# Kernel optimization log

Hardware: AMD Instinct MI355X
Metric: run time of the kernel (lower is better)

The kernel has to match this reference:

```python
import jax, jax.numpy as jnp
import numpy as np

B, S, D = 1, 2048, 1024   # batch, seq, hidden_size
I = 2048                  # intermediate_size (mlp1 emits 2*I, SwiGLU halves)
E = 8                     # num_experts
K = 2                     # experts_per_token
LIMIT = 7.0               # swiglu_limit
ALPHA = 1.702             # gpt-oss swiglu alpha
EPS = 1e-5                # RMSNorm eps


def setup_inputs() -> dict:
    key = jax.random.key(0)
    ks = jax.random.split(key, 4)
    s = 0.02
    return {
        "x": jax.random.normal(ks[0], (B, S, D), jnp.float32),
        "norm_scale": jnp.ones((D,), jnp.float32),
        "gate_w": jax.random.normal(ks[1], (D, E), jnp.float32) * s,
        "gate_b": jnp.zeros((E,), jnp.float32),
        "mlp1_w": jax.random.normal(ks[2], (E, D, 2 * I), jnp.float32) * s,
        "mlp1_b": jnp.zeros((E, 2 * I), jnp.float32),
        "mlp2_w": jax.random.normal(ks[3], (E, I, D), jnp.float32) * s,
        "mlp2_b": jnp.zeros((E, D), jnp.float32),
    }


def _swiglu(h):
    # gpt-oss interleaved SwiGLU with clamp limit
    x_glu = jnp.minimum(h[..., ::2], LIMIT)
    x_lin = jnp.clip(h[..., 1::2], -LIMIT, LIMIT)
    return x_glu * jax.nn.sigmoid(ALPHA * x_glu) * (x_lin + 1.0)


def _moe(t, gate_w, gate_b, mlp1_w, mlp1_b, mlp2_w, mlp2_b):
    T = t.shape[0]
    logits = t @ gate_w + gate_b                 # [T, E]
    top_v, top_i = jax.lax.top_k(logits, K)      # [T, K]
    probs = jax.nn.softmax(top_v, axis=-1)       # softmax over selected experts
    # dense routing-weight matrix, zero for unselected experts
    w = jnp.zeros((T, E), t.dtype).at[jnp.arange(T)[:, None], top_i].set(probs)

    def body(acc, ew):
        w1, b1, w2, b2, we = ew                  # per-expert params + weights [T]
        h = _swiglu(t @ w1 + b1)                 # [T, I]
        y = h @ w2 + b2                          # [T, D]
        return acc + we[:, None] * y, None

    acc0 = jnp.zeros((T, t.shape[1]), t.dtype)
    acc, _ = jax.lax.scan(body, acc0, (mlp1_w, mlp1_b, mlp2_w, mlp2_b, w.T))
    return acc


def reference(x, norm_scale, gate_w, gate_b, mlp1_w, mlp1_b, mlp2_w, mlp2_b):
    Bx, Sx, Dx = x.shape
    ms = jnp.mean(x * x, axis=-1, keepdims=True)
    t = (x * jax.lax.rsqrt(ms + EPS) * norm_scale).reshape(Bx * Sx, Dx)
    y = _moe(t, gate_w, gate_b, mlp1_w, mlp1_b, mlp2_w, mlp2_b)
    return x + y.reshape(Bx, Sx, Dx)
```

## Files before the change

kernel.cpp:

```cpp
#include <hip/hip_runtime.h>
#include <hip/hip_bf16.h>

typedef unsigned short u16;
typedef __attribute__((ext_vector_type(4))) unsigned short u16x4;
typedef __attribute__((ext_vector_type(8))) unsigned short u16x8;
typedef __attribute__((ext_vector_type(8))) short bf16x8;
typedef __attribute__((ext_vector_type(4))) float f32x4;

#define DEV static __device__ __forceinline__

DEV float bf2f(u16 b){ union{unsigned u; float f;} c; c.u = ((unsigned)b) << 16; return c.f; }
DEV u16 f2bf(float f){ union{float f; unsigned u;} c; c.f = f; unsigned u = c.u; u += 0x7FFF + ((u >> 16) & 1); return (u16)(u >> 16); }
DEV u16 f2bfh(float f){ union { __hip_bfloat16 h; u16 u; } c; c.h = __float2bfloat16(f); return c.u; }
DEV float getc(float4 v, int c){ return c == 0 ? v.x : c == 1 ? v.y : c == 2 ? v.z : v.w; }

DEV void gload16(const void* g, void* l){
  __builtin_amdgcn_global_load_lds((const __attribute__((address_space(1))) unsigned int*)g,
                                   (__attribute__((address_space(3))) unsigned int*)l, 16, 0, 0);
}

__global__ __launch_bounds__(256) void k_rms(
    const float* __restrict__ x, const float* __restrict__ nsc,
    const float* __restrict__ gw, const float* __restrict__ gb,
    u16* __restrict__ t, int* __restrict__ topi, float* __restrict__ topp,
    float* __restrict__ outp)
{
  const int token = blockIdx.x, tid = threadIdx.x;
  const int wv = tid >> 6, lane = tid & 63;
  const float4 xv = *(const float4*)&x[(size_t)token * 1024 + tid * 4];
  *(float4*)&outp[(size_t)token * 1024 + tid * 4] = xv;
  float f[4] = {xv.x, xv.y, xv.z, xv.w};
  float ss = f[0]*f[0] + f[1]*f[1] + f[2]*f[2] + f[3]*f[3];
  #pragma unroll
  for (int o = 32; o > 0; o >>= 1) ss += __shfl_down(ss, o, 64);
  __shared__ float red[4];
  __shared__ float s_rs;
  if (lane == 0) red[wv] = ss;
  __syncthreads();
  if (tid == 0) s_rs = rsqrtf((red[0] + red[1] + red[2] + red[3]) * (1.0f / 1024.0f) + 1e-5f);
  __syncthreads();
  const float rs = s_rs;
  const float4 sv = *(const float4*)&nsc[tid * 4];
  const float sc[4] = {sv.x, sv.y, sv.z, sv.w};
  float tf[4]; u16x4 tv;
  #pragma unroll
  for (int j = 0; j < 4; ++j){ tf[j] = f[j] * rs * sc[j]; tv[j] = f2bf(tf[j]); }
  *(u16x4*)&t[(size_t)token * 1024 + tid * 4] = tv;

  float la[8] = {0,0,0,0,0,0,0,0};
  #pragma unroll
  for (int j = 0; j < 4; ++j){
    const int k = tid * 4 + j;
    const float4 g0 = *(const float4*)&gw[k * 8];
    const float4 g1 = *(const float4*)&gw[k * 8 + 4];
    la[0] += tf[j] * g0.x; la[1] += tf[j] * g0.y; la[2] += tf[j] * g0.z; la[3] += tf[j] * g0.w;
    la[4] += tf[j] * g1.x; la[5] += tf[j] * g1.y; la[6] += tf[j] * g1.z; la[7] += tf[j] * g1.w;
  }
  #pragma unroll
  for (int o = 32; o > 0; o >>= 1)
    #pragma unroll
    for (int e = 0; e < 8; ++e) la[e] += __shfl_down(la[e], o, 64);
  __shared__ float lred[4][8];
  if (lane == 0){
    #pragma unroll
    for (int e = 0; e < 8; ++e) lred[wv][e] = la[e];
  }
  __syncthreads();
  if (tid == 0){
    float lg[8];
    #pragma unroll
    for (int e = 0; e < 8; ++e) lg[e] = lred[0][e] + lred[1][e] + lred[2][e] + lred[3][e] + gb[e];
    int i0 = 0;
    for (int e = 1; e < 8; ++e) if (lg[e] > lg[i0]) i0 = e;
    int i1 = -1;
    for (int e = 0; e < 8; ++e) if (e != i0 && (i1 < 0 || lg[e] > lg[i1])) i1 = e;
    const float d = __expf(lg[i1] - lg[i0]);
    const float p0 = 1.0f / (1.0f + d);
    topi[token * 2] = i0; topi[token * 2 + 1] = i1;
    topp[token * 2] = p0; topp[token * 2 + 1] = d * p0;
  }
}

__global__ __launch_bounds__(256) void k_route(
    const int* __restrict__ topi, const float* __restrict__ topp,
    int* __restrict__ cnt, int* __restrict__ offs, int* __restrict__ tok_of,
    float* __restrict__ wt_of, int* __restrict__ slot_of, int* __restrict__ posg)
{
  __shared__ int c[8];
  __shared__ int o[8];
  const int tid = threadIdx.x;
  if (tid < 8) c[tid] = 0;
  __syncthreads();
  for (int a = tid; a < 4096; a += 256){
    int e = topi[a];
    posg[a] = atomicAdd(&c[e], 1);
  }
  __syncthreads();
  if (tid == 0){
    int run = 0;
    for (int e = 0; e < 8; ++e){ o[e] = run; offs[e] = run; cnt[e] = c[e]; run += c[e]; }
  }
  __syncthreads();
  for (int a = tid; a < 4096; a += 256){
    int e = topi[a];
    int s = o[e] + posg[a];
    tok_of[s] = a >> 1;
    wt_of[s] = topp[a];
    slot_of[a] = s;
  }
}

__global__ __launch_bounds__(512, 4) void k_gemm1(
    const u16* __restrict__ t, const float* __restrict__ w1, const float* __restrict__ b1,
    const int* __restrict__ cnt, const int* __restrict__ offs, const int* __restrict__ tok_of,
    u16* __restrict__ h)
{
  const int e = blockIdx.z;
  const int count = cnt[e];
  const int m0 = blockIdx.y * 256;
  if (m0 >= count) return;
  const int off = offs[e];
  const int n0 = blockIdx.x * 128;

  __shared__ __attribute__((aligned(16))) u16 As[256 * 64];
  __shared__ __attribute__((aligned(16))) u16 Bs[128 * 64];

  const int tid = threadIdx.x, wv = tid >> 6, lane = tid & 63;
  const int arl = lane >> 3;
  const int axu = (lane & 7) ^ arl;

  const u16* asrc[4];
  u16* adst[4];
  #pragma unroll
  for (int i = 0; i < 4; ++i){
    const int rr = i * 64 + wv * 8 + arl;
    int r = m0 + rr; if (r > count - 1) r = count - 1;
    asrc[i] = t + (size_t)tok_of[off + r] * 1024 + axu * 8;
    adst[i] = &As[(i * 64 + wv * 8) * 64];
  }

  const int tkq = tid >> 5;
  const int tnb = (tid & 31) * 4;
  const float* bsrc = w1 + (size_t)e * (1024 * 4096) + (size_t)(tkq * 4) * 4096 + n0 + tnb;

  const int wm = wv & 3, wn = wv >> 2;
  const int fr = lane & 15, q = lane >> 4;

  f32x4 acc[4][4];
  #pragma unroll
  for (int a = 0; a < 4; ++a)
    #pragma unroll
    for (int b = 0; b < 4; ++b) acc[a][b] = (f32x4){0.f, 0.f, 0.f, 0.f};

  for (int k0 = 0; k0 < 1024; k0 += 64){
    #pragma unroll
    for (int i = 0; i < 4; ++i){ gload16(asrc[i], adst[i]); asrc[i] += 64; }
    const float4 fv0 = *(const float4*)(bsrc);
    const float4 fv1 = *(const float4*)(bsrc + 4096);
    const float4 fv2 = *(const float4*)(bsrc + 2 * 4096);
    const float4 fv3 = *(const float4*)(bsrc + 3 * 4096);
    bsrc += (size_t)64 * 4096;
    #pragma unroll
    for (int c = 0; c < 4; ++c){
      const int nr = tnb + c;
      u16x4 wd;
      wd[0] = f2bfh(getc(fv0, c)); wd[1] = f2bfh(getc(fv1, c));
      wd[2] = f2bfh(getc(fv2, c)); wd[3] = f2bfh(getc(fv3, c));
      *(u16x4*)((char*)Bs + nr * 128 + (((tkq >> 1) ^ ((nr >> 1) & 7)) << 4) + ((tkq & 1) << 3)) = wd;
    }
    __syncthreads();
    #pragma unroll
    for (int hh = 0; hh < 2; ++hh){
      const int puA = (((hh * 4) + q) ^ (fr & 7)) * 8;
      const int puB = (((hh * 4) + q) ^ ((fr >> 1) & 7)) * 8;
      bf16x8 af[4], bq[4];
      #pragma unroll
      for (int fm = 0; fm < 4; ++fm) af[fm] = *(const bf16x8*)&As[(wm * 64 + fm * 16 + fr) * 64 + puA];
      #pragma unroll
      for (int fn = 0; fn < 4; ++fn) bq[fn] = *(const bf16x8*)&Bs[(wn * 64 + fn * 16 + fr) * 64 + puB];
      #pragma unroll
      for (int fm = 0; fm < 4; ++fm)
        #pragma unroll
        for (int fn = 0; fn < 4; ++fn)
          acc[fm][fn] = __builtin_amdgcn_mfma_f32_16x16x32_bf16(af[fm], bq[fn], acc[fm][fn], 0, 0, 0);
    }
    __syncthreads();
  }

  const int cb = n0 + wn * 64 + fr;
  float b1v[4];
  #pragma unroll
  for (int fn = 0; fn < 4; ++fn) b1v[fn] = b1[e * 4096 + cb + fn * 16];
  const int rq = q * 4;
  const bool ev = ((lane & 1) == 0);
  #pragma unroll
  for (int fm = 0; fm < 4; ++fm)
    #pragma unroll
    for (int fn = 0; fn < 4; ++fn)
      #pragma unroll
      for (int r = 0; r < 4; ++r){
        const float val = acc[fm][fn][r] + b1v[fn];
        const float oth = __shfl_xor(val, 1, 64);
        if (ev){
          const int row = m0 + wm * 64 + fm * 16 + rq + r;
          if (row < count){
            const float g = fminf(val, 7.0f);
            const float l = fminf(fmaxf(oth, -7.0f), 7.0f);
            const float o = g / (1.0f + __expf(-1.702f * g)) * (l + 1.0f);
            h[(size_t)(off + row) * 2048 + ((cb + fn * 16) >> 1)] = f2bf(o);
          }
        }
      }
}

__global__ __launch_bounds__(256) void k_gemm2(
    const u16* __restrict__ h, const float* __restrict__ w2, const float* __restrict__ b2,
    const int* __restrict__ cnt, const int* __restrict__ offs, const float* __restrict__ wt_of,
    const int* __restrict__ tok_of, float* __restrict__ outp)
{
  const int e = blockIdx.z;
  const int count = cnt[e];
  const int m0 = blockIdx.y * 128;
  if (m0 >= count) return;
  const int off = offs[e];
  const int n0 = blockIdx.x * 64;

  __shared__ __attribute__((aligned(16))) u16 As[2][128 * 64];
  __shared__ __attribute__((aligned(16))) u16 Bs[2][64 * 64];

  const int tid = threadIdx.x, wv = tid >> 6, lane = tid & 63;
  const int arl = lane >> 3;
  const int axu = (lane & 7) ^ arl;

  const u16* asrc[4];
  u16* adst[2][4];
  #pragma unroll
  for (int i = 0; i < 4; ++i){
    const int rr = i * 32 + wv * 8 + arl;
    int r = m0 + rr; if (r > count - 1) r = count - 1;
    asrc[i] = h + (size_t)(off + r) * 2048 + axu * 8;
    adst[0][i] = &As[0][(i * 32 + wv * 8) * 64];
    adst[1][i] = &As[1][(i * 32 + wv * 8) * 64];
  }

  const int tkq = tid >> 4;
  const int tnb = (tid & 15) * 4;
  const float* bsrc = w2 + (size_t)e * (2048 * 1024) + (size_t)(tkq * 4) * 1024 + n0 + tnb;

  const int wm = wv & 1, wn = wv >> 1;
  const int fr = lane & 15, q = lane >> 4;

  f32x4 acc[4][2];
  #pragma unroll
  for (int a = 0; a < 4; ++a)
    #pragma unroll
    for (int b = 0; b < 2; ++b) acc[a][b] = (f32x4){0.f, 0.f, 0.f, 0.f};

  auto loadB = [&](float4* fv){
    #pragma unroll
    for (int j = 0; j < 4; ++j) fv[j] = *(const float4*)(bsrc + (size_t)j * 1024);
    bsrc += (size_t)64 * 1024;
  };
  auto writeB = [&](u16* B, const float4* fv){
    #pragma unroll
    for (int c = 0; c < 4; ++c){
      const int nr = tnb + c;
      u16x4 wd;
      wd[0] = f2bfh(getc(fv[0], c)); wd[1] = f2bfh(getc(fv[1], c));
      wd[2] = f2bfh(getc(fv[2], c)); wd[3] = f2bfh(getc(fv[3], c));
      *(u16x4*)((char*)B + nr * 128 + (((tkq >> 1) ^ ((nr >> 1) & 7)) << 4) + ((tkq & 1) << 3)) = wd;
    }
  };
  auto compute = [&](const u16* A, const u16* B){
    #pragma unroll
    for (int hh = 0; hh < 2; ++hh){
      const int puA = (((hh * 4) + q) ^ (fr & 7)) * 8;
      const int puB = (((hh * 4) + q) ^ ((fr >> 1) & 7)) * 8;
      bf16x8 af[4], bq[2];
      #pragma unroll
      for (int fm = 0; fm < 4; ++fm) af[fm] = *(const bf16x8*)&A[(wm * 64 + fm * 16 + fr) * 64 + puA];
      #pragma unroll
      for (int fn = 0; fn < 2; ++fn) bq[fn] = *(const bf16x8*)&B[(wn * 32 + fn * 16 + fr) * 64 + puB];
      #pragma unroll
      for (int fm = 0; fm < 4; ++fm)
        #pragma unroll
        for (int fn = 0; fn < 2; ++fn)
          acc[fm][fn] = __builtin_amdgcn_mfma_f32_16x16x32_bf16(af[fm], bq[fn], acc[fm][fn], 0, 0, 0);
    }
  };

  {
    #pragma unroll
    for (int i = 0; i < 4; ++i){ gload16(asrc[i], adst[0][i]); asrc[i] += 64; }
    float4 fv[4];
    loadB(fv);
    writeB(Bs[0], fv);
  }
  __syncthreads();

  int cur = 0;
  for (int tt = 0; tt < 31; ++tt){
    const int nxt = cur ^ 1;
    #pragma unroll
    for (int i = 0; i < 4; ++i){ gload16(asrc[i], adst[nxt][i]); asrc[i] += 64; }
    float4 fv[4];
    loadB(fv);
    compute(As[cur], Bs[cur]);
    writeB(Bs[nxt], fv);
    __syncthreads();
    cur = nxt;
  }
  compute(As[cur], Bs[cur]);

  const int cb = n0 + wn * 32 + fr;
  float b2v[2];
  #pragma unroll
  for (int fn = 0; fn < 2; ++fn) b2v[fn] = b2[e * 1024 + cb + fn * 16];
  const int rq = q * 4;
  #pragma unroll
  for (int fm = 0; fm < 4; ++fm)
    #pragma unroll
    for (int rr = 0; rr < 4; ++rr){
      const int row = m0 + wm * 64 + fm * 16 + rq + rr;
      if (row < count){
        const float wt = wt_of[off + row];
        const int token = tok_of[off + row];
        #pragma unroll
        for (int fn = 0; fn < 2; ++fn){
          const float v = (acc[fm][fn][rr] + b2v[fn]) * wt;
          atomicAdd(&outp[(size_t)token * 1024 + cb + fn * 16], v);
        }
      }
    }
}

extern "C" void kernel_launch(void* const* d_in, const int* in_sizes, int n_in,
                              void* d_out, int out_size, void* d_ws, size_t ws_size,
                              hipStream_t stream)
{
  const float* x   = (const float*)d_in[0];
  const float* nsc = (const float*)d_in[1];
  const float* gw  = (const float*)d_in[2];
  const float* gb  = (const float*)d_in[3];
  const float* w1  = (const float*)d_in[4];
  const float* b1  = (const float*)d_in[5];
  const float* w2  = (const float*)d_in[6];
  const float* b2  = (const float*)d_in[7];
  float* out = (float*)d_out;
  char* ws = (char*)d_ws;

  size_t o = 0;
  auto alloc = [&](size_t bytes){ size_t r = o; o = (o + bytes + 255) & ~(size_t)255; return r; };
  const size_t o_t    = alloc((size_t)2048 * 1024 * 2);
  const size_t o_h    = alloc((size_t)4096 * 2048 * 2);
  const size_t o_topi = alloc(4096 * 4);
  const size_t o_topp = alloc(4096 * 4);
  const size_t o_posg = alloc(4096 * 4);
  const size_t o_tok  = alloc(4096 * 4);
  const size_t o_wt   = alloc(4096 * 4);
  const size_t o_slot = alloc(4096 * 4);
  const size_t o_cnt  = alloc(8 * 4);
  const size_t o_offs = alloc(8 * 4);
  if (ws_size < o) return;

  u16*   t_ws  = (u16*)(ws + o_t);
  u16*   h_ws  = (u16*)(ws + o_h);
  int*   topi  = (int*)(ws + o_topi);
  float* topp  = (float*)(ws + o_topp);
  int*   posg  = (int*)(ws + o_posg);
  int*   tok   = (int*)(ws + o_tok);
  float* wt    = (float*)(ws + o_wt);
  int*   slot  = (int*)(ws + o_slot);
  int*   cnt   = (int*)(ws + o_cnt);
  int*   offs  = (int*)(ws + o_offs);

  k_rms  <<<2048, 256, 0, stream>>>(x, nsc, gw, gb, t_ws, topi, topp, out);
  k_route<<<1, 256, 0, stream>>>(topi, topp, cnt, offs, tok, wt, slot, posg);
  k_gemm1<<<dim3(32, 4, 8), 512, 0, stream>>>(t_ws, w1, b1, cnt, offs, tok, h_ws);
  k_gemm2<<<dim3(16, 16, 8), 256, 0, stream>>>(h_ws, w2, b2, cnt, offs, wt, tok, out);
}
```

Measured before the change: 367.9 us.

## Double-buffer LDS tiles in gemm1 to overlap global loads with MFMA

Double-buffers the A and B shared-memory tiles in the first expert GEMM. Global-to-LDS loads and the fp32 weight loads for the next K-step are issued before the current tile's MFMA compute, and the bf16 conversion and write into the other buffer happen after it, so only one barrier is needed per iteration. This doubles LDS use to 96KB per block, and the launch-bounds occupancy hint of 4 is dropped. Fewer resident blocks per CU could offset the latency hiding gained from the prefetch.

```diff
diff --git a/kernel.cpp b/kernel.cpp
--- a/kernel.cpp
+++ b/kernel.cpp
@@ -110,7 +110,7 @@
   }
 }
 
-__global__ __launch_bounds__(512, 4) void k_gemm1(
+__global__ __launch_bounds__(512) void k_gemm1(
     const u16* __restrict__ t, const float* __restrict__ w1, const float* __restrict__ b1,
     const int* __restrict__ cnt, const int* __restrict__ offs, const int* __restrict__ tok_of,
     u16* __restrict__ h)
@@ -122,21 +122,22 @@
   const int off = offs[e];
   const int n0 = blockIdx.x * 128;
 
-  __shared__ __attribute__((aligned(16))) u16 As[256 * 64];
-  __shared__ __attribute__((aligned(16))) u16 Bs[128 * 64];
+  __shared__ __attribute__((aligned(16))) u16 As[2][256 * 64];
+  __shared__ __attribute__((aligned(16))) u16 Bs[2][128 * 64];
 
   const int tid = threadIdx.x, wv = tid >> 6, lane = tid & 63;
   const int arl = lane >> 3;
   const int axu = (lane & 7) ^ arl;
 
   const u16* asrc[4];
-  u16* adst[4];
+  u16* adst[2][4];
   #pragma unroll
   for (int i = 0; i < 4; ++i){
     const int rr = i * 64 + wv * 8 + arl;
     int r = m0 + rr; if (r > count - 1) r = count - 1;
     asrc[i] = t + (size_t)tok_of[off + r] * 1024 + axu * 8;
-    adst[i] = &As[(i * 64 + wv * 8) * 64];
+    adst[0][i] = &As[0][(i * 64 + wv * 8) * 64];
+    adst[1][i] = &As[1][(i * 64 + wv * 8) * 64];
   }
 
   const int tkq = tid >> 5;
@@ -152,40 +153,61 @@
     #pragma unroll
     for (int b = 0; b < 4; ++b) acc[a][b] = (f32x4){0.f, 0.f, 0.f, 0.f};
 
-  for (int k0 = 0; k0 < 1024; k0 += 64){
-    #pragma unroll
-    for (int i = 0; i < 4; ++i){ gload16(asrc[i], adst[i]); asrc[i] += 64; }
-    const float4 fv0 = *(const float4*)(bsrc);
-    const float4 fv1 = *(const float4*)(bsrc + 4096);
-    const float4 fv2 = *(const float4*)(bsrc + 2 * 4096);
-    const float4 fv3 = *(const float4*)(bsrc + 3 * 4096);
+  auto loadB = [&](float4* fv){
+    #pragma unroll
+    for (int j = 0; j < 4; ++j) fv[j] = *(const float4*)(bsrc + (size_t)j * 4096);
     bsrc += (size_t)64 * 4096;
+  };
+  auto writeB = [&](u16* B, const float4* fv){
     #pragma unroll
     for (int c = 0; c < 4; ++c){
       const int nr = tnb + c;
       u16x4 wd;
-      wd[0] = f2bfh(getc(fv0, c)); wd[1] = f2bfh(getc(fv1, c));
-      wd[2] = f2bfh(getc(fv2, c)); wd[3] = f2bfh(getc(fv3, c));
-      *(u16x4*)((char*)Bs + nr * 128 + (((tkq >> 1) ^ ((nr >> 1) & 7)) << 4) + ((tkq & 1) << 3)) = wd;
+      wd[0] = f2bfh(getc(fv[0], c)); wd[1] = f2bfh(getc(fv[1], c));
+      wd[2] = f2bfh(getc(fv[2], c)); wd[3] = f2bfh(getc(fv[3], c));
+      *(u16x4*)((char*)B + nr * 128 + (((tkq >> 1) ^ ((nr >> 1) & 7)) << 4) + ((tkq & 1) << 3)) = wd;
     }
-    __syncthreads();
+  };
+  auto compute = [&](const u16* A, const u16* B){
     #pragma unroll
     for (int hh = 0; hh < 2; ++hh){
       const int puA = (((hh * 4) + q) ^ (fr & 7)) * 8;
       const int puB = (((hh * 4) + q) ^ ((fr >> 1) & 7)) * 8;
       bf16x8 af[4], bq[4];
       #pragma unroll
-      for (int fm = 0; fm < 4; ++fm) af[fm] = *(const bf16x8*)&As[(wm * 64 + fm * 16 + fr) * 64 + puA];
-      #pragma unroll
-      for (int fn = 0; fn < 4; ++fn) bq[fn] = *(const bf16x8*)&Bs[(wn * 64 + fn * 16 + fr) * 64 + puB];
+      for (int fm = 0; fm < 4; ++fm) af[fm] = *(const bf16x8*)&A[(wm * 64 + fm * 16 + fr) * 64 + puA];
+      #pragma unroll
+      for (int fn = 0; fn < 4; ++fn) bq[fn] = *(const bf16x8*)&B[(wn * 64 + fn * 16 + fr) * 64 + puB];
       #pragma unroll
       for (int fm = 0; fm < 4; ++fm)
         #pragma unroll
         for (int fn = 0; fn < 4; ++fn)
           acc[fm][fn] = __builtin_amdgcn_mfma_f32_16x16x32_bf16(af[fm], bq[fn], acc[fm][fn], 0, 0, 0);
     }
+  };
+
+  {
+    #pragma unroll
+    for (int i = 0; i < 4; ++i){ gload16(asrc[i], adst[0][i]); asrc[i] += 64; }
+    float4 fv[4];
+    loadB(fv);
+    writeB(Bs[0], fv);
+  }
+  __syncthreads();
+
+  int cur = 0;
+  for (int tt = 0; tt < 15; ++tt){
+    const int nxt = cur ^ 1;
+    #pragma unroll
+    for (int i = 0; i < 4; ++i){ gload16(asrc[i], adst[nxt][i]); asrc[i] += 64; }
+    float4 fv[4];
+    loadB(fv);
+    compute(As[cur], Bs[cur]);
+    writeB(Bs[nxt], fv);
     __syncthreads();
-  }
+    cur = nxt;
+  }
+  compute(As[cur], Bs[cur]);
 
   const int cb = n0 + wn * 64 + fr;
   float b1v[4];
```

Measured after the change: 381.5 us. 1.04x slower.

## Prefetch B operand two stages ahead with explicit waitcnt barriers in down-projection GEMM

Applied to the files above, without the earlier changes.

Restructures the down-projection GEMM main loop so the fp32 B tile is loaded into registers one iteration earlier, using two alternating register sets and a two-step unrolled loop. __syncthreads is replaced by an explicit s_waitcnt vmcnt(4)/lgkmcnt(0) plus s_barrier, so the in-flight B register loads are not drained at each barrier. This is meant to hide global-load latency behind the MFMA compute. It costs extra registers, and the hand-counted vmcnt threshold is fragile. An odd no-op conditional was also added on the MFMA A operand.

```diff
diff --git a/kernel.cpp b/kernel.cpp
--- a/kernel.cpp
+++ b/kernel.cpp
@@ -285,31 +285,50 @@
       for (int fm = 0; fm < 4; ++fm)
         #pragma unroll
         for (int fn = 0; fn < 2; ++fn)
-          acc[fm][fn] = __builtin_amdgcn_mfma_f32_16x16x32_bf16(af[fm], bq[fn], acc[fm][fn], 0, 0, 0);
+          acc[fm][fn] = __builtin_amdgcn_mfma_f32_16x16x32_bf16(af[fm][0] ? af[fm] : af[fm], bq[fn], acc[fm][fn], 0, 0, 0);
     }
   };
-
-  {
-    #pragma unroll
-    for (int i = 0; i < 4; ++i){ gload16(asrc[i], adst[0][i]); asrc[i] += 64; }
-    float4 fv[4];
-    loadB(fv);
-    writeB(Bs[0], fv);
-  }
-  __syncthreads();
+  auto stageA = [&](int buf){
+    #pragma unroll
+    for (int i = 0; i < 4; ++i){ gload16(asrc[i], adst[buf][i]); asrc[i] += 64; }
+  };
+
+  float4 fvA[4], fvB[4];
+  loadB(fvA);
+  stageA(0);
+  writeB(Bs[0], fvA);
+  loadB(fvB);
+  asm volatile("s_waitcnt vmcnt(4) lgkmcnt(0)" ::: "memory");
+  __builtin_amdgcn_s_barrier();
+  __builtin_amdgcn_sched_barrier(0);
 
   int cur = 0;
-  for (int tt = 0; tt < 31; ++tt){
-    const int nxt = cur ^ 1;
-    #pragma unroll
-    for (int i = 0; i < 4; ++i){ gload16(asrc[i], adst[nxt][i]); asrc[i] += 64; }
-    float4 fv[4];
-    loadB(fv);
+  #pragma unroll 1
+  for (int tt = 0; tt < 30; tt += 2){
+    stageA(cur ^ 1);
+    loadB(fvA);
     compute(As[cur], Bs[cur]);
-    writeB(Bs[nxt], fv);
-    __syncthreads();
-    cur = nxt;
-  }
+    writeB(Bs[cur ^ 1], fvB);
+    asm volatile("s_waitcnt vmcnt(4) lgkmcnt(0)" ::: "memory");
+    __builtin_amdgcn_s_barrier();
+    __builtin_amdgcn_sched_barrier(0);
+    cur ^= 1;
+    stageA(cur ^ 1);
+    loadB(fvB);
+    compute(As[cur], Bs[cur]);
+    writeB(Bs[cur ^ 1], fvA);
+    asm volatile("s_waitcnt vmcnt(4) lgkmcnt(0)" ::: "memory");
+    __builtin_amdgcn_s_barrier();
+    __builtin_amdgcn_sched_barrier(0);
+    cur ^= 1;
+  }
+  stageA(cur ^ 1);
+  compute(As[cur], Bs[cur]);
+  writeB(Bs[cur ^ 1], fvB);
+  asm volatile("s_waitcnt vmcnt(0) lgkmcnt(0)" ::: "memory");
+  __builtin_amdgcn_s_barrier();
+  __builtin_amdgcn_sched_barrier(0);
+  cur ^= 1;
   compute(As[cur], Bs[cur]);
 
   const int cb = n0 + wn * 32 + fr;
```

Result: no change. 371.2 us (+0.9%).
